# Performance work log

Hardware: AMD Instinct MI355X
Metric: run time of the kernel (lower is better)

## Reference

```python
import jax, jax.numpy as jnp
import numpy as np
import math

B, H, S, D = 4, 16, 1024, 64
NEG = -1000000000.0

def setup_inputs() -> dict:
    key = jax.random.key(0)
    ks = jax.random.split(key, 6)
    return {
        "query": jax.random.normal(ks[0], (B, H, S, D), dtype=jnp.float32),
        "key": jax.random.normal(ks[1], (B, H, S, D), dtype=jnp.float32),
        "value": jax.random.normal(ks[2], (B, H, S, D), dtype=jnp.float32),
        "head_nums": H,
        "mask": jax.random.randint(ks[3], (B, S), 0, 2, dtype=jnp.int32),
        "topic_query": jax.random.normal(ks[4], (B, S, D), dtype=jnp.float32),
        "topic_key": jax.random.normal(ks[5], (B, S, D), dtype=jnp.float32),
    }

def reference(query, key, value, head_nums, mask, topic_query, topic_key):
    d = query.shape[-1]
    # scores: [B,H,S,S]
    scores = jnp.einsum("bhqd,bhkd->bhqk", query, key) / math.sqrt(d)
    # pairwise mask: [B,S,S] (mask_i * mask_j)
    pair_mask = (mask[:, :, None] * mask[:, None, :]) != 0
    scores = jnp.where(pair_mask[:, None, :, :], scores, NEG)
    # topic modulation: per-token (no head dim), broadcast over heads
    dt = topic_query.shape[-1]
    topic_scores = jnp.einsum("bqd,bkd->bqk", topic_query, topic_key) / math.sqrt(dt)
    topic_scores = jnp.where(pair_mask, topic_scores, 1.0)[:, None, :, :]  # [B,1,S,S]
    topic_probs = jax.nn.softmax(topic_scores, axis=-1)
    scores = scores * topic_probs
    p_attn = jax.nn.softmax(scores, axis=-1)
    out = jnp.einsum("bhqk,bhkd->bhqd", p_attn, value)
    return (out, p_attn)
```

## Files before the change

### kernel.cpp

```cpp
#include <hip/hip_runtime.h>

#define B_ 4
#define H_ 16
#define S_ 1024
#define D_ 64
#define NEGV -1000000000.0f

typedef __bf16 bf16x8 __attribute__((ext_vector_type(8)));
typedef __bf16 bf16x4 __attribute__((ext_vector_type(4)));
typedef float f32x4 __attribute__((ext_vector_type(4)));

#define MFMA16(A, B, C) __builtin_amdgcn_mfma_f32_16x16x32_bf16(A, B, C, 0, 0, 0)

__device__ __forceinline__ void bar_lds() {
  asm volatile("s_waitcnt lgkmcnt(0)" ::: "memory");
  __builtin_amdgcn_sched_barrier(0);
  __builtin_amdgcn_s_barrier();
  __builtin_amdgcn_sched_barrier(0);
}

__device__ __forceinline__ bf16x8 cvt8(const float* p) {
  float4 x = *(const float4*)p;
  float4 y = *(const float4*)(p + 4);
  bf16x8 f;
  f[0]=(__bf16)x.x; f[1]=(__bf16)x.y; f[2]=(__bf16)x.z; f[3]=(__bf16)x.w;
  f[4]=(__bf16)y.x; f[5]=(__bf16)y.y; f[6]=(__bf16)y.z; f[7]=(__bf16)y.w;
  return f;
}

__global__ __launch_bounds__(256) void prep_kernel(
    const float* __restrict__ K, const float* __restrict__ V,
    __bf16* __restrict__ Kb, __bf16* __restrict__ Vt)
{
  int bid = blockIdx.x;
  int sc = bid & 15;
  int bh = bid >> 4;
  int tid = threadIdx.x;
  __shared__ float s_v[64][65];

  const float* Kc = K + ((size_t)bh*S_ + sc*64)*D_;
  const float* Vc = V + ((size_t)bh*S_ + sc*64)*D_;
  __bf16* Kbc = Kb + ((size_t)bh*S_ + sc*64)*D_;

  {
    const float4* src = (const float4*)Kc + tid*4;
    float4 a = src[0], b = src[1], c = src[2], d = src[3];
    bf16x8 o0, o1;
    o0[0]=(__bf16)a.x; o0[1]=(__bf16)a.y; o0[2]=(__bf16)a.z; o0[3]=(__bf16)a.w;
    o0[4]=(__bf16)b.x; o0[5]=(__bf16)b.y; o0[6]=(__bf16)b.z; o0[7]=(__bf16)b.w;
    o1[0]=(__bf16)c.x; o1[1]=(__bf16)c.y; o1[2]=(__bf16)c.z; o1[3]=(__bf16)c.w;
    o1[4]=(__bf16)d.x; o1[5]=(__bf16)d.y; o1[6]=(__bf16)d.z; o1[7]=(__bf16)d.w;
    *(bf16x8*)(Kbc + tid*16)     = o0;
    *(bf16x8*)(Kbc + tid*16 + 8) = o1;
  }
  for (int i = tid; i < 64*16; i += 256) {
    int r = i >> 4, c4 = i & 15;
    float4 v = ((const float4*)(Vc + (size_t)r*D_))[c4];
    s_v[r][c4*4+0] = v.x; s_v[r][c4*4+1] = v.y;
    s_v[r][c4*4+2] = v.z; s_v[r][c4*4+3] = v.w;
  }
  __syncthreads();
  {
    int d = tid >> 2, seg = tid & 3;
    bf16x8 o0, o1;
    #pragma unroll
    for (int j = 0; j < 8; ++j) o0[j] = (__bf16)s_v[seg*16 + j][d];
    #pragma unroll
    for (int j = 0; j < 8; ++j) o1[j] = (__bf16)s_v[seg*16 + 8 + j][d];
    __bf16* dst = Vt + ((size_t)bh*D_ + d)*S_ + sc*64 + seg*16;
    *(bf16x8*)dst = o0;
    *(bf16x8*)(dst + 8) = o1;
  }
}

__global__ __launch_bounds__(256) void topic_kernel(
    const float* __restrict__ tq, const float* __restrict__ tk,
    const int* __restrict__ mask, __bf16* __restrict__ tp)
{
  int bid0 = blockIdx.x;
  int bid = (bid0 & 7)*32 + (bid0 >> 3);
  int qt = bid & 63, b = bid >> 6;
  int tid = threadIdx.x, wave = tid >> 6, lane = tid & 63;
  int l15 = lane & 15, lhi = lane >> 4;
  __shared__ float2 s_red[4][16];
  __shared__ __align__(16) char s_mem[4*8704];

  const int* mb = mask + b*S_;
  bf16x8 qf[2];
  #pragma unroll
  for (int dc = 0; dc < 2; ++dc)
    qf[dc] = cvt8(tq + ((size_t)b*S_ + qt*16 + l15)*D_ + dc*32 + lhi*8);
  int mq = mb[qt*16 + l15];

  f32x4 sc[16];
  #pragma unroll
  for (int kt = 0; kt < 16; ++kt) {
    int kb = wave*256 + kt*16;
    const float* kr = tk + ((size_t)b*S_ + kb + l15)*D_ + lhi*8;
    bf16x8 k0 = cvt8(kr);
    bf16x8 k1 = cvt8(kr + 32);
    f32x4 acc = {0.f,0.f,0.f,0.f};
    acc = MFMA16(k0, qf[0], acc);
    acc = MFMA16(k1, qf[1], acc);
    int4 mk = *(const int4*)(mb + kb + lhi*4);
    sc[kt][0] = (mq && mk.x) ? acc[0]*0.125f : 1.0f;
    sc[kt][1] = (mq && mk.y) ? acc[1]*0.125f : 1.0f;
    sc[kt][2] = (mq && mk.z) ? acc[2]*0.125f : 1.0f;
    sc[kt][3] = (mq && mk.w) ? acc[3]*0.125f : 1.0f;
  }
  float m = -3.4e38f;
  #pragma unroll
  for (int kt = 0; kt < 16; ++kt)
    #pragma unroll
    for (int i = 0; i < 4; ++i) m = fmaxf(m, sc[kt][i]);
  m = fmaxf(m, __shfl_xor(m, 16));
  m = fmaxf(m, __shfl_xor(m, 32));
  float sum = 0.f;
  #pragma unroll
  for (int kt = 0; kt < 16; ++kt)
    #pragma unroll
    for (int i = 0; i < 4; ++i) { sc[kt][i] = __expf(sc[kt][i] - m); sum += sc[kt][i]; }
  sum += __shfl_xor(sum, 16);
  sum += __shfl_xor(sum, 32);
  if (lane < 16) s_red[wave][l15] = make_float2(m, sum);
  bar_lds();
  float M = -3.4e38f;
  #pragma unroll
  for (int w = 0; w < 4; ++w) M = fmaxf(M, s_red[w][l15].x);
  float Z = 0.f;
  #pragma unroll
  for (int w = 0; w < 4; ++w) Z += s_red[w][l15].y * __expf(s_red[w][l15].x - M);
  float scale = __expf(m - M) / Z;

  #pragma unroll
  for (int kt = 0; kt < 16; ++kt) {
    int kb = wave*256 + kt*16;
    int4 mk = *(const int4*)(mb + kb + lhi*4);
    sc[kt][0] *= scale; if (!(mq && mk.x)) sc[kt][0] = -sc[kt][0];
    sc[kt][1] *= scale; if (!(mq && mk.y)) sc[kt][1] = -sc[kt][1];
    sc[kt][2] *= scale; if (!(mq && mk.z)) sc[kt][2] = -sc[kt][2];
    sc[kt][3] *= scale; if (!(mq && mk.w)) sc[kt][3] = -sc[kt][3];
  }

  float* xw = (float*)s_mem + wave*2176;
  __bf16* tpw = tp + ((size_t)b*S_ + qt*16)*S_ + wave*256;
  #pragma unroll
  for (int h = 0; h < 2; ++h) {
    #pragma unroll
    for (int j = 0; j < 8; ++j)
      *(f32x4*)(xw + l15*136 + j*16 + lhi*4) = sc[h*8 + j];
    bar_lds();
    #pragma unroll
    for (int rr = 0; rr < 8; ++rr) {
      int r = rr*2 + (lane >> 5);
      f32x4 a = *(f32x4*)(xw + r*136 + (lane & 31)*4);
      bf16x4 o;
      o[0]=(__bf16)a[0]; o[1]=(__bf16)a[1]; o[2]=(__bf16)a[2]; o[3]=(__bf16)a[3];
      *(bf16x4*)(tpw + (size_t)r*S_ + h*128 + (lane & 31)*4) = o;
    }
    bar_lds();
  }
}

__global__ __launch_bounds__(256) void attn_kernel(
    const float* __restrict__ Q, const __bf16* __restrict__ Kb,
    const __bf16* __restrict__ Vt, const __bf16* __restrict__ tp,
    float* __restrict__ out, float* __restrict__ pa)
{
  int bid0 = blockIdx.x;
  int bid = (bid0 & 7)*512 + (bid0 >> 3);
  int qt = bid & 63;
  int h  = (bid >> 6) & 15;
  int b  = bid >> 10;
  int tid = threadIdx.x, wave = tid >> 6, lane = tid & 63;
  int l15 = lane & 15, lhi = lane >> 4;

  __shared__ __align__(16) char s_p[16*2048];

  size_t bh = (size_t)b*H_ + h;
  const __bf16* Kbh = Kb + bh*S_*D_;
  const __bf16* tpb = tp + ((size_t)b*S_ + qt*16)*S_;

  bf16x8 qf[2];
  #pragma unroll
  for (int dc = 0; dc < 2; ++dc)
    qf[dc] = cvt8(Q + (bh*S_ + qt*16 + l15)*D_ + dc*32 + lhi*8);

  for (int kt = 0; kt < 16; ++kt) {
    int kb = wave*256 + kt*16;
    int kcol = kb + l15;
    const __bf16* kr = Kbh + (size_t)kcol*D_ + lhi*8;
    bf16x8 k0 = *(const bf16x8*)kr;
    bf16x8 k1 = *(const bf16x8*)(kr + 32);
    f32x4 acc = {0.f,0.f,0.f,0.f};
    acc = MFMA16(qf[0], k0, acc);
    acc = MFMA16(qf[1], k1, acc);
    #pragma unroll
    for (int i = 0; i < 4; ++i) {
      int row = lhi*4 + i;
      float t = (float)tpb[(size_t)row*S_ + kcol];
      float s = (t > 0.f) ? acc[i]*0.125f*t : NEGV*(-t);
      *(__bf16*)(s_p + row*2048 + ((kcol*2) ^ ((row&7)<<4))) = (__bf16)s;
    }
  }
  bar_lds();

  #pragma unroll
  for (int r = 0; r < 4; ++r) {
    int row = wave*4 + r;
    int swz = (row & 7) << 4;
    float sv[16]; float m = -3.4e38f;
    #pragma unroll
    for (int j = 0; j < 16; ++j) {
      sv[j] = (float)*(const __bf16*)(s_p + row*2048 + (((lane + j*64)*2) ^ swz));
      m = fmaxf(m, sv[j]);
    }
    #pragma unroll
    for (int o = 32; o >= 1; o >>= 1) m = fmaxf(m, __shfl_xor(m, o));
    float ev[16]; float sum = 0.f;
    #pragma unroll
    for (int j = 0; j < 16; ++j) { ev[j] = __expf(sv[j]-m); sum += ev[j]; }
    #pragma unroll
    for (int o = 32; o >= 1; o >>= 1) sum += __shfl_xor(sum, o);
    float inv = 1.0f/sum;
    float* par = pa + (bh*S_ + qt*16 + row)*S_;
    #pragma unroll
    for (int j = 0; j < 16; ++j) {
      float pv = ev[j]*inv;
      par[lane + j*64] = pv;
      *(__bf16*)(s_p + row*2048 + (((lane + j*64)*2) ^ swz)) = (__bf16)pv;
    }
  }
  bar_lds();

  const __bf16* Vh = Vt + (bh*D_ + wave*16 + l15)*S_ + lhi*8;
  f32x4 oacc = {0.f,0.f,0.f,0.f};
  #pragma unroll 8
  for (int ks = 0; ks < 32; ++ks) {
    bf16x8 a  = *(const bf16x8*)(s_p + l15*2048 + ((ks*64 + lhi*16) ^ ((l15 & 7) << 4)));
    bf16x8 bv = *(const bf16x8*)(Vh + ks*32);
    oacc = MFMA16(a, bv, oacc);
  }
  #pragma unroll
  for (int i = 0; i < 4; ++i)
    out[(bh*S_ + qt*16 + lhi*4 + i)*D_ + wave*16 + l15] = oacc[i];
}

extern "C" void kernel_launch(void* const* d_in, const int* in_sizes, int n_in,
                              void* d_out, int out_size, void* d_ws, size_t ws_size,
                              hipStream_t stream) {
  const float* Q    = (const float*)d_in[0];
  const float* K    = (const float*)d_in[1];
  const float* V    = (const float*)d_in[2];
  const int*   mask = (const int*)d_in[4];
  const float* tq   = (const float*)d_in[5];
  const float* tk   = (const float*)d_in[6];

  __bf16* tp = (__bf16*)d_ws;
  __bf16* Kb = tp + (size_t)B_*S_*S_;
  __bf16* Vt = Kb + (size_t)B_*H_*S_*D_;

  float* outp = (float*)d_out;
  float* pa   = outp + (size_t)B_*H_*S_*D_;

  prep_kernel <<<B_*H_*16, 256, 0, stream>>>(K, V, Kb, Vt);
  topic_kernel<<<B_*64,    256, 0, stream>>>(tq, tk, mask, tp);
  attn_kernel <<<B_*H_*64, 256, 0, stream>>>(Q, Kb, Vt, tp, outp, pa);
}
```

Baseline: 182.8 us.

## Fuse online softmax statistics into QK loop and prefetch K/V into registers

The QK^T loop now keeps a running per-row max and rescaled sum while it produces scores. A cross-lane and cross-wave reduction through a small shared array replaces the separate max and sum passes, so the softmax phase does one read/exp/write pass per row instead of two. K tiles and V tiles are also loaded two iterations ahead into a three-entry register ring to hide global load latency behind the MFMAs. In exchange, the online update costs roughly two extra exponentials per score. The ring buffers are indexed modulo 3, which could spill to scratch if the loops are not fully unrolled.

```diff
diff --git a/kernel.cpp b/kernel.cpp
--- a/kernel.cpp
+++ b/kernel.cpp
@@ -176,6 +176,7 @@
   int l15 = lane & 15, lhi = lane >> 4;
 
   __shared__ __align__(16) char s_p[16*2048];
+  __shared__ float2 s_red[4][16];
 
   size_t bh = (size_t)b*H_ + h;
   const __bf16* Kbh = Kb + bh*S_*D_;
@@ -186,47 +187,71 @@
   for (int dc = 0; dc < 2; ++dc)
     qf[dc] = cvt8(Q + (bh*S_ + qt*16 + l15)*D_ + dc*32 + lhi*8);
 
+  f32x4 pm = {-3.4e38f,-3.4e38f,-3.4e38f,-3.4e38f};
+  f32x4 pz = {0.f,0.f,0.f,0.f};
+  bf16x8 rk0[3], rk1[3];
+  #pragma unroll
+  for (int p = 0; p < 2; ++p) {
+    const __bf16* kr = Kbh + (size_t)(wave*256 + p*16 + l15)*D_ + lhi*8;
+    rk0[p] = *(const bf16x8*)kr;
+    rk1[p] = *(const bf16x8*)(kr + 32);
+  }
   for (int kt = 0; kt < 16; ++kt) {
-    int kb = wave*256 + kt*16;
-    int kcol = kb + l15;
-    const __bf16* kr = Kbh + (size_t)kcol*D_ + lhi*8;
-    bf16x8 k0 = *(const bf16x8*)kr;
-    bf16x8 k1 = *(const bf16x8*)(kr + 32);
+    const int cur = kt % 3;
+    if (kt + 2 < 16) {
+      const int nxt = (kt + 2) % 3;
+      const __bf16* kr = Kbh + (size_t)(wave*256 + (kt+2)*16 + l15)*D_ + lhi*8;
+      rk0[nxt] = *(const bf16x8*)kr;
+      rk1[nxt] = *(const bf16x8*)(kr + 32);
+    }
+    int kcol = wave*256 + kt*16 + l15;
     f32x4 acc = {0.f,0.f,0.f,0.f};
-    acc = MFMA16(qf[0], k0, acc);
-    acc = MFMA16(qf[1], k1, acc);
+    acc = MFMA16(qf[0], rk0[cur], acc);
+    acc = MFMA16(qf[1], rk1[cur], acc);
     #pragma unroll
     for (int i = 0; i < 4; ++i) {
       int row = lhi*4 + i;
       float t = (float)tpb[(size_t)row*S_ + kcol];
       float s = (t > 0.f) ? acc[i]*0.125f*t : NEGV*(-t);
       *(__bf16*)(s_p + row*2048 + ((kcol*2) ^ ((row&7)<<4))) = (__bf16)s;
-    }
+      float sB = (float)(__bf16)s;
+      float nm = fmaxf(pm[i], sB);
+      pz[i] = pz[i]*__expf(pm[i]-nm) + __expf(sB-nm);
+      pm[i] = nm;
+    }
+  }
+  #pragma unroll
+  for (int o = 1; o <= 8; o <<= 1) {
+    #pragma unroll
+    for (int i = 0; i < 4; ++i) {
+      float mo = __shfl_xor(pm[i], o);
+      float zo = __shfl_xor(pz[i], o);
+      float nm = fmaxf(pm[i], mo);
+      pz[i] = pz[i]*__expf(pm[i]-nm) + zo*__expf(mo-nm);
+      pm[i] = nm;
+    }
+  }
+  if (l15 == 0) {
+    #pragma unroll
+    for (int i = 0; i < 4; ++i)
+      s_red[wave][lhi*4 + i] = make_float2(pm[i], pz[i]);
   }
   bar_lds();
 
   #pragma unroll
   for (int r = 0; r < 4; ++r) {
     int row = wave*4 + r;
+    float2 a0 = s_red[0][row], a1 = s_red[1][row], a2 = s_red[2][row], a3 = s_red[3][row];
+    float M = fmaxf(fmaxf(a0.x, a1.x), fmaxf(a2.x, a3.x));
+    float Z = a0.y*__expf(a0.x-M) + a1.y*__expf(a1.x-M)
+            + a2.y*__expf(a2.x-M) + a3.y*__expf(a3.x-M);
+    float inv = 1.0f / Z;
     int swz = (row & 7) << 4;
-    float sv[16]; float m = -3.4e38f;
+    float* par = pa + (bh*S_ + qt*16 + row)*S_;
     #pragma unroll
     for (int j = 0; j < 16; ++j) {
-      sv[j] = (float)*(const __bf16*)(s_p + row*2048 + (((lane + j*64)*2) ^ swz));
-      m = fmaxf(m, sv[j]);
-    }
-    #pragma unroll
-    for (int o = 32; o >= 1; o >>= 1) m = fmaxf(m, __shfl_xor(m, o));
-    float ev[16]; float sum = 0.f;
-    #pragma unroll
-    for (int j = 0; j < 16; ++j) { ev[j] = __expf(sv[j]-m); sum += ev[j]; }
-    #pragma unroll
-    for (int o = 32; o >= 1; o >>= 1) sum += __shfl_xor(sum, o);
-    float inv = 1.0f/sum;
-    float* par = pa + (bh*S_ + qt*16 + row)*S_;
-    #pragma unroll
-    for (int j = 0; j < 16; ++j) {
-      float pv = ev[j]*inv;
+      float sv = (float)*(const __bf16*)(s_p + row*2048 + (((lane + j*64)*2) ^ swz));
+      float pv = __expf(sv - M) * inv;
       par[lane + j*64] = pv;
       *(__bf16*)(s_p + row*2048 + (((lane + j*64)*2) ^ swz)) = (__bf16)pv;
     }
@@ -234,12 +259,14 @@
   bar_lds();
 
   const __bf16* Vh = Vt + (bh*D_ + wave*16 + l15)*S_ + lhi*8;
+  bf16x8 rv[3];
+  #pragma unroll
+  for (int p = 0; p < 2; ++p) rv[p] = *(const bf16x8*)(Vh + p*32);
   f32x4 oacc = {0.f,0.f,0.f,0.f};
-  #pragma unroll 8
   for (int ks = 0; ks < 32; ++ks) {
-    bf16x8 a  = *(const bf16x8*)(s_p + l15*2048 + ((ks*64 + lhi*16) ^ ((l15 & 7) << 4)));
-    bf16x8 bv = *(const bf16x8*)(Vh + ks*32);
-    oacc = MFMA16(a, bv, oacc);
+    if (ks + 2 < 32) rv[(ks+2)%3] = *(const bf16x8*)(Vh + (ks+2)*32);
+    bf16x8 a = *(const bf16x8*)(s_p + l15*2048 + ((ks*64 + lhi*16) ^ ((l15 & 7) << 4)));
+    oacc = MFMA16(a, rv[ks%3], oacc);
   }
   #pragma unroll
   for (int i = 0; i < 4; ++i)
```

New measurement: 510.7 us. 179% more time.
